# Optimization experiments

Measured on AMD Instinct MI355X. Metric: run time of the kernel, lower is better.

The kernel has to match this reference:

```python
import jax, jax.numpy as jnp
import numpy as np

N_HOPS = 2

def _l2norm(x, eps=1e-8):
    # torch F.normalize: x / norm.clamp_min(eps)
    n = jnp.linalg.norm(x, axis=-1, keepdims=True)
    return x / jnp.maximum(n, eps)

def setup_inputs() -> dict:
    key = jax.random.key(0)
    ks = jax.random.split(key, 6)
    Nu, Ne, R, E, d = 100000, 100000, 64, 600000, 128
    # scale 0.3 keeps attention logits small enough that exp() stays finite in fp32
    user_embedding = jax.random.normal(ks[0], (Nu, d), jnp.float32) * 0.3
    relation_embedding = jax.random.normal(ks[1], (R, d), jnp.float32) * 0.3
    entity_emb = jax.random.normal(ks[2], (Ne, d), jnp.float32) * 0.3
    # xavier_uniform with relu gain: bound = sqrt(2)*sqrt(6/(2d+d))
    bound = np.sqrt(2.0) * np.sqrt(6.0 / (2 * d + d))
    W = jax.random.uniform(ks[3], (2 * d, d), jnp.float32, -bound, bound)
    edge_index = jax.random.randint(ks[4], (2, E), 0, Nu, jnp.int32)
    edge_type = jax.random.randint(ks[5], (E,), 0, R, jnp.int32)
    return {"user_embedding": user_embedding, "relation_embedding": relation_embedding,
            "entity_emb": entity_emb, "W": W, "edge_index": edge_index, "edge_type": edge_type}

def reference(user_embedding, relation_embedding, entity_emb, W, edge_index, edge_type):
    head, tail = edge_index[0], edge_index[1]
    Nu = user_embedding.shape[0]
    Ne = entity_emb.shape[0]
    rel_e = relation_embedding[edge_type]  # [E, d]
    usr_all = user_embedding
    ent_all = entity_emb
    for _ in range(N_HOPS):
        h_u = usr_all[head]            # [E, d]
        t_e = ent_all[tail]            # [E, d]
        a = jnp.concatenate([h_u, t_e], axis=-1)          # [E, 2d]
        e = jnp.sum((a @ W) * rel_e, axis=-1)             # [E]
        e = jnp.where(e > 0, e, 0.2 * e)                  # LeakyReLU(0.2)
        e_exp = jnp.exp(e)
        # segment softmax grouped by head (denominator detached as in original)
        denom_u = jax.lax.stop_gradient(
            jax.ops.segment_sum(e_exp, head, num_segments=Nu))[head]
        e_user = e_exp / denom_u
        agg_u = jax.ops.segment_sum(t_e * e_user[:, None], head, num_segments=Nu)
        agg_u = agg_u + usr_all
        # segment softmax grouped by tail
        denom_i = jax.lax.stop_gradient(
            jax.ops.segment_sum(e_exp, tail, num_segments=Ne))[tail]
        e_item = e_exp / denom_i
        agg_i = jax.ops.segment_sum(h_u * e_item[:, None], tail, num_segments=Ne)
        agg_i = agg_i + ent_all
        # eval mode: dropout disabled (identity)
        agg_i = _l2norm(agg_i)
        agg_u = _l2norm(agg_u)
        ent_all = ent_all + agg_i
        usr_all = usr_all + agg_u
    return usr_all, ent_all
```

## Files before the change

kernel.cpp:

```cpp
#include <hip/hip_runtime.h>
#include <hip/hip_bf16.h>

#define D 128
#define NB 16

__global__ __launch_bounds__(256) void compute_wr(const float* __restrict__ W,
                                                  const float* __restrict__ rel,
                                                  float* __restrict__ wrT) {
    int r = blockIdx.x;
    int m = threadIdx.x;
    const float4* wrow = (const float4*)(W + (size_t)m * D);
    const float4* rrow = (const float4*)(rel + (size_t)r * D);
    float s = 0.f;
#pragma unroll
    for (int k = 0; k < D / 4; ++k) {
        float4 a = wrow[k];
        float4 b = rrow[k];
        s += a.x * b.x + a.y * b.y + a.z * b.z + a.w * b.w;
    }
    wrT[(size_t)m * 64 + r] = s;
}

__global__ __launch_bounds__(256) void count_deg(const int* __restrict__ head,
                                                 const int* __restrict__ tail,
                                                 int* __restrict__ deg_u,
                                                 int* __restrict__ deg_i, int E) {
    int e = blockIdx.x * 256 + threadIdx.x;
    if (e >= E) return;
    atomicAdd(deg_u + head[e], 1);
    atomicAdd(deg_i + tail[e], 1);
}

__global__ __launch_bounds__(1024) void scan_bsum(const int* __restrict__ deg,
                                                  int* __restrict__ bsum, int N) {
    __shared__ int lds[1024];
    int b = blockIdx.x, tid = threadIdx.x;
    int base = b * 4096 + tid * 4;
    int s = 0;
#pragma unroll
    for (int j = 0; j < 4; ++j) { int i = base + j; if (i < N) s += deg[i]; }
    lds[tid] = s;
    __syncthreads();
    for (int off = 1; off < 1024; off <<= 1) {
        int t = (tid >= off) ? lds[tid - off] : 0;
        __syncthreads();
        lds[tid] += t;
        __syncthreads();
    }
    if (tid == 1023) bsum[b] = lds[1023];
}

__global__ __launch_bounds__(64) void scan_off(const int* __restrict__ bsum,
                                               int* __restrict__ boff, int nb) {
    int tid = threadIdx.x;
    int v = (tid < nb) ? bsum[tid] : 0;
    int incl = v;
    for (int off = 1; off < 64; off <<= 1) {
        int t = __shfl_up(incl, off, 64);
        if (tid >= off) incl += t;
    }
    if (tid < nb) boff[tid] = incl - v;
    if (tid == 63) boff[nb] = incl;
}

__global__ __launch_bounds__(1024) void scan_write(const int* __restrict__ deg,
                                                   const int* __restrict__ boff,
                                                   int* __restrict__ rowptr,
                                                   int* __restrict__ cur, int N, int nb) {
    __shared__ int lds[1024];
    int b = blockIdx.x, tid = threadIdx.x;
    int base = b * 4096 + tid * 4;
    int v[4];
    int s = 0;
#pragma unroll
    for (int j = 0; j < 4; ++j) { int i = base + j; v[j] = (i < N) ? deg[i] : 0; s += v[j]; }
    lds[tid] = s;
    __syncthreads();
    for (int off = 1; off < 1024; off <<= 1) {
        int t = (tid >= off) ? lds[tid - off] : 0;
        __syncthreads();
        lds[tid] += t;
        __syncthreads();
    }
    int run = boff[b] + lds[tid] - s;
#pragma unroll
    for (int j = 0; j < 4; ++j) {
        int i = base + j;
        if (i < N) { rowptr[i] = run; cur[i] = run; run += v[j]; }
    }
    if (b == 0 && tid == 0) rowptr[N] = boff[nb];
}

__global__ __launch_bounds__(256) void fill_adj(const int* __restrict__ head,
                                                const int* __restrict__ tail,
                                                int* __restrict__ cur_u,
                                                int* __restrict__ cur_i,
                                                int* __restrict__ adj_u,
                                                int* __restrict__ adj_i,
                                                int* __restrict__ pos_u,
                                                int* __restrict__ pos_i, int E) {
    int e = blockIdx.x * 256 + threadIdx.x;
    if (e >= E) return;
    int h = head[e], t = tail[e];
    int su = atomicAdd(cur_u + h, 1);
    adj_u[su] = t;
    pos_u[e] = su;
    int si = atomicAdd(cur_i + t, 1);
    adj_i[si] = h;
    pos_i[e] = si;
}

__global__ __launch_bounds__(256, 3) void node_tables(const float* __restrict__ rows,
                                                      const float* __restrict__ wrT,
                                                      float* __restrict__ out, int N) {
    int lane = threadIdx.x & 63;
    int wave = threadIdx.x >> 6;
    float w[128];
#pragma unroll
    for (int kk = 0; kk < 128; ++kk) w[kk] = wrT[(size_t)kk * 64 + lane];

    __shared__ float lds[NB * D];

    int ngroups = (N + NB - 1) / NB;
    int g = blockIdx.x;
    if (g >= ngroups) return;

    int i0 = threadIdx.x;
    int i1 = threadIdx.x + 256;

    float4 v0, v1;
    {
        const float4* gsrc = (const float4*)(rows + (size_t)g * NB * D);
        int maxslot = min(N - g * NB, NB) * (D / 4);
        v0 = (i0 < maxslot) ? gsrc[i0] : make_float4(0.f, 0.f, 0.f, 0.f);
        v1 = (i1 < maxslot) ? gsrc[i1] : make_float4(0.f, 0.f, 0.f, 0.f);
    }
    while (true) {
        ((float4*)lds)[i0] = v0;
        ((float4*)lds)[i1] = v1;
        __syncthreads();
        int gn = g + gridDim.x;
        if (gn < ngroups) {
            const float4* gsrc = (const float4*)(rows + (size_t)gn * NB * D);
            int maxslot = min(N - gn * NB, NB) * (D / 4);
            v0 = (i0 < maxslot) ? gsrc[i0] : make_float4(0.f, 0.f, 0.f, 0.f);
            v1 = (i1 < maxslot) ? gsrc[i1] : make_float4(0.f, 0.f, 0.f, 0.f);
        }
        int n0 = g * NB;
#pragma unroll
        for (int i = 0; i < 4; ++i) {
            int nl = wave * 4 + i;
            const float4* rp = (const float4*)(lds + nl * D);
            float a0 = 0.f, a1 = 0.f, a2 = 0.f, a3 = 0.f;
#pragma unroll
            for (int j = 0; j < 32; ++j) {
                float4 v = rp[j];
                a0 += v.x * w[4 * j + 0];
                a1 += v.y * w[4 * j + 1];
                a2 += v.z * w[4 * j + 2];
                a3 += v.w * w[4 * j + 3];
            }
            int n = n0 + nl;
            if (n < N) out[(size_t)n * 64 + lane] = (a0 + a1) + (a2 + a3);
        }
        if (gn >= ngroups) break;
        __syncthreads();
        g = gn;
    }
}

__global__ __launch_bounds__(256) void edge_weights(const int* __restrict__ head,
                                                    const int* __restrict__ tail,
                                                    const int* __restrict__ etype,
                                                    const int* __restrict__ pos_u,
                                                    const int* __restrict__ pos_i,
                                                    const float* __restrict__ alpha,
                                                    const float* __restrict__ beta,
                                                    float* __restrict__ ew_u,
                                                    float* __restrict__ ew_i, int E) {
    int e = blockIdx.x * 256 + threadIdx.x;
    if (e >= E) return;
    int h = head[e], t = tail[e], r = etype[e];
    float s = alpha[(size_t)h * 64 + r] + beta[(size_t)t * 64 + r];
    s = s > 0.f ? s : 0.2f * s;
    float ex = expf(s);
    ew_u[pos_u[e]] = ex;
    ew_i[pos_i[e]] = ex;
}

__global__ __launch_bounds__(256) void agg_nodes(const float* __restrict__ src_rows,
                                                 const float* __restrict__ self_rows,
                                                 const float* __restrict__ ew,
                                                 const int* __restrict__ rowptr,
                                                 const int* __restrict__ adj_src,
                                                 float* __restrict__ dst, int N) {
    int node = (int)((blockIdx.x * (size_t)blockDim.x + threadIdx.x) >> 6);
    int lane = threadIdx.x & 63;
    if (node >= N) return;
    int beg = rowptr[node];
    int end = rowptr[node + 1];
    float ax = 0.f, ay = 0.f, esum = 0.f;
    int p = beg;
    float w_cur = 0.f;
    float2 v_cur = make_float2(0.f, 0.f);
    if (p < end) {
        w_cur = ew[p];
        v_cur = ((const float2*)(src_rows + (size_t)adj_src[p] * D))[lane];
    }
    while (p < end) {
        int pn = p + 1;
        float w_n = 0.f;
        float2 v_n = make_float2(0.f, 0.f);
        if (pn < end) {
            w_n = ew[pn];
            v_n = ((const float2*)(src_rows + (size_t)adj_src[pn] * D))[lane];
        }
        ax += w_cur * v_cur.x;
        ay += w_cur * v_cur.y;
        esum += w_cur;
        w_cur = w_n;
        v_cur = v_n;
        p = pn;
    }
    float inv_e = (end > beg) ? 1.f / esum : 0.f;
    float2 self = ((const float2*)(self_rows + (size_t)node * D))[lane];
    float gx = ax * inv_e + self.x;
    float gy = ay * inv_e + self.y;
    float n2 = gx * gx + gy * gy;
#pragma unroll
    for (int off = 32; off; off >>= 1) n2 += __shfl_xor(n2, off, 64);
    float inv = 1.f / fmaxf(sqrtf(n2), 1e-8f);
    float2 o;
    o.x = self.x + gx * inv;
    o.y = self.y + gy * inv;
    ((float2*)(dst + (size_t)node * D))[lane] = o;
}

extern "C" void kernel_launch(void* const* d_in, const int* in_sizes, int n_in,
                              void* d_out, int out_size, void* d_ws, size_t ws_size,
                              hipStream_t stream) {
    const float* user = (const float*)d_in[0];
    const float* rel  = (const float*)d_in[1];
    const float* ent  = (const float*)d_in[2];
    const float* W    = (const float*)d_in[3];
    const int* eidx   = (const int*)d_in[4];
    const int* etype  = (const int*)d_in[5];

    int Nu = in_sizes[0] / D;
    int R  = in_sizes[1] / D;
    int Ne = in_sizes[2] / D;
    int E  = in_sizes[5];
    const int* head = eidx;
    const int* tail = eidx + E;

    float* out_usr = (float*)d_out;
    float* out_ent = out_usr + (size_t)Nu * D;

    float* alpha = (float*)d_out;
    float* beta  = alpha + (size_t)Nu * 64;

    float* fp = (float*)d_ws;
    float* usr_ws = fp; fp += (size_t)Nu * D;
    float* ent_ws = fp; fp += (size_t)Ne * D;
    float* ew_u   = fp; fp += E;
    float* ew_i   = fp; fp += E;
    float* wrT    = fp; fp += (size_t)2 * D * 64;
    int* ip = (int*)fp;
    int* deg_u    = ip; ip += Nu;
    int* deg_i    = ip; ip += Ne;
    int* cur_u    = ip; ip += Nu;
    int* cur_i    = ip; ip += Ne;
    int* rowptr_u = ip; ip += Nu + 1;
    int* rowptr_i = ip; ip += Ne + 1;
    int* adj_u    = ip; ip += E;
    int* adj_i    = ip; ip += E;
    int* pos_u    = ip; ip += E;
    int* pos_i    = ip; ip += E;
    int* bsum_u   = ip; ip += 64;
    int* bsum_i   = ip; ip += 64;
    int* boff_u   = ip; ip += 65;
    int* boff_i   = ip; ip += 65;

    int nb_u = (Nu + 4095) / 4096;
    int nb_i = (Ne + 4095) / 4096;

    hipMemsetAsync(deg_u, 0, (size_t)(Nu + Ne) * sizeof(int), stream);
    compute_wr<<<R, 256, 0, stream>>>(W, rel, wrT);
    count_deg<<<(E + 255) / 256, 256, 0, stream>>>(head, tail, deg_u, deg_i, E);
    scan_bsum<<<nb_u, 1024, 0, stream>>>(deg_u, bsum_u, Nu);
    scan_off<<<1, 64, 0, stream>>>(bsum_u, boff_u, nb_u);
    scan_write<<<nb_u, 1024, 0, stream>>>(deg_u, boff_u, rowptr_u, cur_u, Nu, nb_u);
    scan_bsum<<<nb_i, 1024, 0, stream>>>(deg_i, bsum_i, Ne);
    scan_off<<<1, 64, 0, stream>>>(bsum_i, boff_i, nb_i);
    scan_write<<<nb_i, 1024, 0, stream>>>(deg_i, boff_i, rowptr_i, cur_i, Ne, nb_i);
    fill_adj<<<(E + 255) / 256, 256, 0, stream>>>(head, tail, cur_u, cur_i,
                                                  adj_u, adj_i, pos_u, pos_i, E);

    int eb = (E + 255) / 256;

    node_tables<<<768, 256, 0, stream>>>(user, wrT, alpha, Nu);
    node_tables<<<768, 256, 0, stream>>>(ent, wrT + (size_t)D * 64, beta, Ne);
    edge_weights<<<eb, 256, 0, stream>>>(head, tail, etype, pos_u, pos_i,
                                         alpha, beta, ew_u, ew_i, E);
    agg_nodes<<<(Nu + 3) / 4, 256, 0, stream>>>(ent, user, ew_u, rowptr_u, adj_u,
                                                usr_ws, Nu);
    agg_nodes<<<(Ne + 3) / 4, 256, 0, stream>>>(user, ent, ew_i, rowptr_i, adj_i,
                                                ent_ws, Ne);

    node_tables<<<768, 256, 0, stream>>>(usr_ws, wrT, alpha, Nu);
    node_tables<<<768, 256, 0, stream>>>(ent_ws, wrT + (size_t)D * 64, beta, Ne);
    edge_weights<<<eb, 256, 0, stream>>>(head, tail, etype, pos_u, pos_i,
                                         alpha, beta, ew_u, ew_i, E);
    agg_nodes<<<(Nu + 3) / 4, 256, 0, stream>>>(ent_ws, usr_ws, ew_u, rowptr_u, adj_u,
                                                out_usr, Nu);
    agg_nodes<<<(Ne + 3) / 4, 256, 0, stream>>>(usr_ws, ent_ws, ew_i, rowptr_i, adj_i,
                                                out_ent, Ne);
}
```

Before: 984.5 us.

## Merge user and entity CSR into one graph and process two edges per wave

Builds a single combined CSR over users and entities. Adjacency entries become (neighbor, edge id) pairs, so edge weights are written once in edge order instead of being scattered through position arrays. The aggregation kernel runs over both node types in one launch, and each wave splits into two half-waves that each load a different edge with float4 loads, then combine results with a cross-half shuffle. This removes the pos arrays, the duplicated scans and launches, and the scattered ew writes, at the cost of an extra indirection through the edge id for each weight and wider adjacency entries.

```diff
diff --git a/kernel.cpp b/kernel.cpp
--- a/kernel.cpp
+++ b/kernel.cpp
@@ -23,12 +23,11 @@
 
 __global__ __launch_bounds__(256) void count_deg(const int* __restrict__ head,
                                                  const int* __restrict__ tail,
-                                                 int* __restrict__ deg_u,
-                                                 int* __restrict__ deg_i, int E) {
+                                                 int* __restrict__ deg, int Nu, int E) {
     int e = blockIdx.x * 256 + threadIdx.x;
     if (e >= E) return;
-    atomicAdd(deg_u + head[e], 1);
-    atomicAdd(deg_i + tail[e], 1);
+    atomicAdd(deg + head[e], 1);
+    atomicAdd(deg + Nu + tail[e], 1);
 }
 
 __global__ __launch_bounds__(1024) void scan_bsum(const int* __restrict__ deg,
@@ -93,21 +92,15 @@
 
 __global__ __launch_bounds__(256) void fill_adj(const int* __restrict__ head,
                                                 const int* __restrict__ tail,
-                                                int* __restrict__ cur_u,
-                                                int* __restrict__ cur_i,
-                                                int* __restrict__ adj_u,
-                                                int* __restrict__ adj_i,
-                                                int* __restrict__ pos_u,
-                                                int* __restrict__ pos_i, int E) {
+                                                int* __restrict__ cur,
+                                                int2* __restrict__ adj, int Nu, int E) {
     int e = blockIdx.x * 256 + threadIdx.x;
     if (e >= E) return;
     int h = head[e], t = tail[e];
-    int su = atomicAdd(cur_u + h, 1);
-    adj_u[su] = t;
-    pos_u[e] = su;
-    int si = atomicAdd(cur_i + t, 1);
-    adj_i[si] = h;
-    pos_i[e] = si;
+    int su = atomicAdd(cur + h, 1);
+    adj[su] = make_int2(t, e);
+    int si = atomicAdd(cur + Nu + t, 1);
+    adj[si] = make_int2(h, e);
 }
 
 __global__ __launch_bounds__(256, 3) void node_tables(const float* __restrict__ rows,
@@ -172,68 +165,91 @@
 __global__ __launch_bounds__(256) void edge_weights(const int* __restrict__ head,
                                                     const int* __restrict__ tail,
                                                     const int* __restrict__ etype,
-                                                    const int* __restrict__ pos_u,
-                                                    const int* __restrict__ pos_i,
                                                     const float* __restrict__ alpha,
                                                     const float* __restrict__ beta,
-                                                    float* __restrict__ ew_u,
-                                                    float* __restrict__ ew_i, int E) {
+                                                    float* __restrict__ ew, int E) {
     int e = blockIdx.x * 256 + threadIdx.x;
     if (e >= E) return;
     int h = head[e], t = tail[e], r = etype[e];
     float s = alpha[(size_t)h * 64 + r] + beta[(size_t)t * 64 + r];
     s = s > 0.f ? s : 0.2f * s;
-    float ex = expf(s);
-    ew_u[pos_u[e]] = ex;
-    ew_i[pos_i[e]] = ex;
-}
-
-__global__ __launch_bounds__(256) void agg_nodes(const float* __restrict__ src_rows,
-                                                 const float* __restrict__ self_rows,
+    ew[e] = expf(s);
+}
+
+__global__ __launch_bounds__(256) void agg_nodes(const float* __restrict__ usr_rows,
+                                                 const float* __restrict__ ent_rows,
                                                  const float* __restrict__ ew,
                                                  const int* __restrict__ rowptr,
-                                                 const int* __restrict__ adj_src,
-                                                 float* __restrict__ dst, int N) {
-    int node = (int)((blockIdx.x * (size_t)blockDim.x + threadIdx.x) >> 6);
+                                                 const int2* __restrict__ adj,
+                                                 float* __restrict__ dst_u,
+                                                 float* __restrict__ dst_e,
+                                                 int Nu, int Ntot) {
+    int wid = (int)((blockIdx.x * (size_t)blockDim.x + threadIdx.x) >> 6);
     int lane = threadIdx.x & 63;
-    if (node >= N) return;
-    int beg = rowptr[node];
-    int end = rowptr[node + 1];
-    float ax = 0.f, ay = 0.f, esum = 0.f;
+    if (wid >= Ntot) return;
+    int half = lane >> 5, li = lane & 31;
+    const float* src;
+    const float* self;
+    float* dst;
+    int node;
+    if (wid < Nu) { node = wid;      src = ent_rows; self = usr_rows; dst = dst_u; }
+    else          { node = wid - Nu; src = usr_rows; self = ent_rows; dst = dst_e; }
+    int beg = rowptr[wid], end = rowptr[wid + 1];
+
+    float4 acc = make_float4(0.f, 0.f, 0.f, 0.f);
+    float esum = 0.f;
     int p = beg;
-    float w_cur = 0.f;
-    float2 v_cur = make_float2(0.f, 0.f);
+    float w_c = 0.f;
+    float4 v_c = make_float4(0.f, 0.f, 0.f, 0.f);
     if (p < end) {
-        w_cur = ew[p];
-        v_cur = ((const float2*)(src_rows + (size_t)adj_src[p] * D))[lane];
+        int srcn = 0;
+        int pe = p + half;
+        if (pe < end) { int2 a = adj[pe]; srcn = a.x; w_c = ew[a.y]; }
+        v_c = ((const float4*)(src + (size_t)srcn * D))[li];
     }
     while (p < end) {
-        int pn = p + 1;
+        int pn = p + 2;
         float w_n = 0.f;
-        float2 v_n = make_float2(0.f, 0.f);
+        float4 v_n = make_float4(0.f, 0.f, 0.f, 0.f);
         if (pn < end) {
-            w_n = ew[pn];
-            v_n = ((const float2*)(src_rows + (size_t)adj_src[pn] * D))[lane];
+            int srcn = 0;
+            int pe = pn + half;
+            if (pe < end) { int2 a = adj[pe]; srcn = a.x; w_n = ew[a.y]; }
+            v_n = ((const float4*)(src + (size_t)srcn * D))[li];
         }
-        ax += w_cur * v_cur.x;
-        ay += w_cur * v_cur.y;
-        esum += w_cur;
-        w_cur = w_n;
-        v_cur = v_n;
+        acc.x += w_c * v_c.x;
+        acc.y += w_c * v_c.y;
+        acc.z += w_c * v_c.z;
+        acc.w += w_c * v_c.w;
+        esum += w_c;
+        w_c = w_n;
+        v_c = v_n;
         p = pn;
     }
+    esum += __shfl_xor(esum, 32, 64);
+    acc.x += __shfl_xor(acc.x, 32, 64);
+    acc.y += __shfl_xor(acc.y, 32, 64);
+    acc.z += __shfl_xor(acc.z, 32, 64);
+    acc.w += __shfl_xor(acc.w, 32, 64);
     float inv_e = (end > beg) ? 1.f / esum : 0.f;
-    float2 self = ((const float2*)(self_rows + (size_t)node * D))[lane];
-    float gx = ax * inv_e + self.x;
-    float gy = ay * inv_e + self.y;
-    float n2 = gx * gx + gy * gy;
-#pragma unroll
-    for (int off = 32; off; off >>= 1) n2 += __shfl_xor(n2, off, 64);
+    float4 s4 = ((const float4*)(self + (size_t)node * D))[li];
+    float4 g;
+    g.x = acc.x * inv_e + s4.x;
+    g.y = acc.y * inv_e + s4.y;
+    g.z = acc.z * inv_e + s4.z;
+    g.w = acc.w * inv_e + s4.w;
+    float n2 = g.x * g.x + g.y * g.y + g.z * g.z + g.w * g.w;
+#pragma unroll
+    for (int off = 16; off; off >>= 1) n2 += __shfl_xor(n2, off, 64);
     float inv = 1.f / fmaxf(sqrtf(n2), 1e-8f);
-    float2 o;
-    o.x = self.x + gx * inv;
-    o.y = self.y + gy * inv;
-    ((float2*)(dst + (size_t)node * D))[lane] = o;
+    if (half == 0) {
+        float4 o;
+        o.x = s4.x + g.x * inv;
+        o.y = s4.y + g.y * inv;
+        o.z = s4.z + g.z * inv;
+        o.w = s4.w + g.w * inv;
+        ((float4*)(dst + (size_t)node * D))[li] = o;
+    }
 }
 
 extern "C" void kernel_launch(void* const* d_in, const int* in_sizes, int n_in,
@@ -250,6 +266,7 @@
     int R  = in_sizes[1] / D;
     int Ne = in_sizes[2] / D;
     int E  = in_sizes[5];
+    int Ntot = Nu + Ne;
     const int* head = eidx;
     const int* tail = eidx + E;
 
@@ -262,57 +279,38 @@
     float* fp = (float*)d_ws;
     float* usr_ws = fp; fp += (size_t)Nu * D;
     float* ent_ws = fp; fp += (size_t)Ne * D;
-    float* ew_u   = fp; fp += E;
-    float* ew_i   = fp; fp += E;
+    float* ew     = fp; fp += E;
     float* wrT    = fp; fp += (size_t)2 * D * 64;
     int* ip = (int*)fp;
-    int* deg_u    = ip; ip += Nu;
-    int* deg_i    = ip; ip += Ne;
-    int* cur_u    = ip; ip += Nu;
-    int* cur_i    = ip; ip += Ne;
-    int* rowptr_u = ip; ip += Nu + 1;
-    int* rowptr_i = ip; ip += Ne + 1;
-    int* adj_u    = ip; ip += E;
-    int* adj_i    = ip; ip += E;
-    int* pos_u    = ip; ip += E;
-    int* pos_i    = ip; ip += E;
-    int* bsum_u   = ip; ip += 64;
-    int* bsum_i   = ip; ip += 64;
-    int* boff_u   = ip; ip += 65;
-    int* boff_i   = ip; ip += 65;
-
-    int nb_u = (Nu + 4095) / 4096;
-    int nb_i = (Ne + 4095) / 4096;
-
-    hipMemsetAsync(deg_u, 0, (size_t)(Nu + Ne) * sizeof(int), stream);
+    int* deg    = ip; ip += Ntot;
+    int* cur    = ip; ip += Ntot;
+    int* rowptr = ip; ip += Ntot + 1;
+    int2* adj   = (int2*)ip; ip += 4 * E;
+    int* bsum   = ip; ip += 64;
+    int* boff   = ip; ip += 65;
+
+    int nb = (Ntot + 4095) / 4096;
+
+    hipMemsetAsync(deg, 0, (size_t)Ntot * sizeof(int), stream);
     compute_wr<<<R, 256, 0, stream>>>(W, rel, wrT);
-    count_deg<<<(E + 255) / 256, 256, 0, stream>>>(head, tail, deg_u, deg_i, E);
-    scan_bsum<<<nb_u, 1024, 0, stream>>>(deg_u, bsum_u, Nu);
-    scan_off<<<1, 64, 0, stream>>>(bsum_u, boff_u, nb_u);
-    scan_write<<<nb_u, 1024, 0, stream>>>(deg_u, boff_u, rowptr_u, cur_u, Nu, nb_u);
-    scan_bsum<<<nb_i, 1024, 0, stream>>>(deg_i, bsum_i, Ne);
-    scan_off<<<1, 64, 0, stream>>>(bsum_i, boff_i, nb_i);
-    scan_write<<<nb_i, 1024, 0, stream>>>(deg_i, boff_i, rowptr_i, cur_i, Ne, nb_i);
-    fill_adj<<<(E + 255) / 256, 256, 0, stream>>>(head, tail, cur_u, cur_i,
-                                                  adj_u, adj_i, pos_u, pos_i, E);
+    count_deg<<<(E + 255) / 256, 256, 0, stream>>>(head, tail, deg, Nu, E);
+    scan_bsum<<<nb, 1024, 0, stream>>>(deg, bsum, Ntot);
+    scan_off<<<1, 64, 0, stream>>>(bsum, boff, nb);
+    scan_write<<<nb, 1024, 0, stream>>>(deg, boff, rowptr, cur, Ntot, nb);
+    fill_adj<<<(E + 255) / 256, 256, 0, stream>>>(head, tail, cur, adj, Nu, E);
 
     int eb = (E + 255) / 256;
+    int ab = (Ntot + 3) / 4;
 
     node_tables<<<768, 256, 0, stream>>>(user, wrT, alpha, Nu);
     node_tables<<<768, 256, 0, stream>>>(ent, wrT + (size_t)D * 64, beta, Ne);
-    edge_weights<<<eb, 256, 0, stream>>>(head, tail, etype, pos_u, pos_i,
-                                         alpha, beta, ew_u, ew_i, E);
-    agg_nodes<<<(Nu + 3) / 4, 256, 0, stream>>>(ent, user, ew_u, rowptr_u, adj_u,
-                                                usr_ws, Nu);
-    agg_nodes<<<(Ne + 3) / 4, 256, 0, stream>>>(user, ent, ew_i, rowptr_i, adj_i,
-                                                ent_ws, Ne);
+    edge_weights<<<eb, 256, 0, stream>>>(head, tail, etype, alpha, beta, ew, E);
+    agg_nodes<<<ab, 256, 0, stream>>>(user, ent, ew, rowptr, adj,
+                                      usr_ws, ent_ws, Nu, Ntot);
 
     node_tables<<<768, 256, 0, stream>>>(usr_ws, wrT, alpha, Nu);
     node_tables<<<768, 256, 0, stream>>>(ent_ws, wrT + (size_t)D * 64, beta, Ne);
-    edge_weights<<<eb, 256, 0, stream>>>(head, tail, etype, pos_u, pos_i,
-                                         alpha, beta, ew_u, ew_i, E);
-    agg_nodes<<<(Nu + 3) / 4, 256, 0, stream>>>(ent_ws, usr_ws, ew_u, rowptr_u, adj_u,
-                                                out_usr, Nu);
-    agg_nodes<<<(Ne + 3) / 4, 256, 0, stream>>>(usr_ws, ent_ws, ew_i, rowptr_i, adj_i,
-                                                out_ent, Ne);
-}
+    edge_weights<<<eb, 256, 0, stream>>>(head, tail, etype, alpha, beta, ew, E);
+    agg_nodes<<<ab, 256, 0, stream>>>(usr_ws, ent_ws, ew, rowptr, adj,
+                                      out_usr, out_ent, Nu, Ntot);
+}
```

After: 861.3 us. -12.5%, faster.
